# Kernel tuning notes

Measured on AMD Instinct MI355X. Metric: run time of the kernel, lower is better.

## Reference

```python
import jax, jax.numpy as jnp
import numpy as np

FEATURE_DIM = 128

def setup_inputs() -> dict:
    key0 = jax.random.key(0)
    k1, k2, k3 = jax.random.split(key0, 3)
    B, NQ, NK, D = 4, 4096, 4096, FEATURE_DIM
    return {
        "target": jax.random.normal(k1, (B, NQ, D), dtype=jnp.float32),
        "key": jax.random.normal(k2, (B, NK, D), dtype=jnp.float32),
        "value": jax.random.normal(k3, (B, NK, D), dtype=jnp.float32),
    }

def reference(target, key, value):
    # Lan_K F: scores = target @ key^T / sqrt(d); weights = softmax(scores); out = weights @ value
    scale = 1.0 / np.sqrt(FEATURE_DIM).astype(np.float32)
    scores = jnp.einsum('bqd,bkd->bqk', target, key) * scale  # [B, NQ, NK]
    weights = jax.nn.softmax(scores, axis=-1)
    return jnp.einsum('bqk,bkd->bqd', weights, value)  # [B, NQ, D]
```

## Files before the change

### kernel.cpp

```cpp
#include <hip/hip_runtime.h>
#include <stdint.h>

#define B_ 4
#define NQ_ 4096
#define NK_ 4096
#define D_ 128
#define BM_ 64
#define BN_ 128
#define NITER_ (NK_/BN_)
#define KVBUF_ 33792
#define PS_ 136
#define OS_ 66

typedef __attribute__((ext_vector_type(8))) short short8;
typedef __attribute__((ext_vector_type(4))) float floatx4;
typedef unsigned int u32;

union frag_u { u32 u[4]; short8 s; };
union pair_u { u32 u[2]; uint2 v; };

__device__ __forceinline__ unsigned short f2bf_rne(float x){
  union { float f; u32 u; } c; c.f = x;
  u32 u = c.u;
  return (unsigned short)((u + 0x7fffu + ((u >> 16) & 1u)) >> 16);
}
__device__ __forceinline__ u32 pk2bf(float a, float b){
  union { float f; u32 u; } x, y; x.f = a; y.f = b;
  return ((x.u + 0x8000u) >> 16) | ((y.u + 0x8000u) & 0xffff0000u);
}

#define GLD16(gp, lp) __builtin_amdgcn_global_load_lds( \
    (const __attribute__((address_space(1))) u32*)(gp),  \
    (__attribute__((address_space(3))) u32*)(lp), 16, 0, 0)

#define TS_ 136
__global__ void prep_kernel(const float* __restrict__ k, const float* __restrict__ v,
                            unsigned short* __restrict__ kb, unsigned short* __restrict__ vt){
  if (blockIdx.x >= 256){
    int base = (blockIdx.x - 256) * 2048 + threadIdx.x;
    #pragma unroll
    for (int i = 0; i < 8; i++){
      int j = base + i*256;
      float4 val = ((const float4*)k)[j];
      ushort4 s;
      s.x = f2bf_rne(val.x); s.y = f2bf_rne(val.y);
      s.z = f2bf_rne(val.z); s.w = f2bf_rne(val.w);
      ((ushort4*)kb)[j] = s;
    }
    return;
  }
  __shared__ __align__(16) float tile[64*TS_];
  int blk = blockIdx.x; int b = blk >> 6; int kt = blk & 63; int k0 = kt*64;
  int t = threadIdx.x;
  const float* vb = v + ((size_t)b*NK_ + k0)*D_;
  #pragma unroll
  for (int i=0;i<8;i++){
    int f = t + i*256;
    int row = f >> 5, c4 = f & 31;
    *(float4*)(tile + row*TS_ + c4*4) = *(const float4*)(vb + row*D_ + c4*4);
  }
  __syncthreads();
  unsigned short* vtb = vt + (size_t)b*D_*NK_ + k0;
  #pragma unroll
  for (int i=0;i<16;i++){
    int u2 = t + i*256;
    int d = u2 >> 5, kp = u2 & 31;
    ushort2 s2;
    s2.x = f2bf_rne(tile[(2*kp)*TS_ + d]);
    s2.y = f2bf_rne(tile[(2*kp+1)*TS_ + d]);
    *(ushort2*)(vtb + (size_t)d*NK_ + 2*kp) = s2;
  }
}

__global__ __launch_bounds__(512, 2) void attn_kernel(
    const float* __restrict__ Qf, const unsigned short* __restrict__ Kb,
    const unsigned short* __restrict__ Vt, float* __restrict__ Out){
  __shared__ __align__(16) char sm[154624];
  char* smKb = sm;
  char* smVb = sm + 2*KVBUF_;
  unsigned short* smP = (unsigned short*)(sm + 4*KVBUF_);
  float* smL = (float*)(sm + 4*KVBUF_ + 64*PS_*2);
  float* smO = (float*)sm;

  const int bi = blockIdx.x;
  const int b  = (bi >> 1) & 3;
  const int qt = ((bi >> 3) << 1) | (bi & 1);
  const int q0 = qt * BM_;
  const int tid = threadIdx.x;
  const int w = tid >> 6, lane = tid & 63;
  const int kg = w >> 1, dh = w & 1;
  const int l15 = lane & 15, l4 = lane >> 4;

  const unsigned short* kgb = Kb + (size_t)b * NK_ * D_;
  const unsigned short* vgb = Vt + (size_t)b * D_ * NK_;

  #pragma unroll
  for (int i = 0; i < 4; i++){
    int c = w*4 + i;
    { int kgc = c>>3, cp = c&7;
      int dchunk = kgc*8 + (cp&1)*4 + (cp>>1);
      const unsigned short* g = kgb + (size_t)(kgc*32 + cp*4 + (lane>>4))*D_ + (lane&15)*8;
      GLD16(g, smKb + dchunk*1056); }
    { const unsigned short* g = vgb + (size_t)(c*4 + (lane>>4))*NK_ + (lane&15)*8;
      GLD16(g, smVb + c*1056); }
  }

  short8 qf[4][4];
  {
    const float* qp = Qf + ((size_t)b*NQ_ + q0)*D_;
    #pragma unroll
    for (int nb = 0; nb < 4; nb++)
      #pragma unroll
      for (int kb = 0; kb < 4; kb++){
        const float* p = qp + (size_t)(nb*16 + l15)*D_ + kb*32 + l4*8;
        float4 a = *(const float4*)p;
        float4 c4 = *(const float4*)(p + 4);
        frag_u f;
        f.u[0] = pk2bf(a.x, a.y);  f.u[1] = pk2bf(a.z, a.w);
        f.u[2] = pk2bf(c4.x, c4.y); f.u[3] = pk2bf(c4.z, c4.w);
        qf[nb][kb] = f.s;
      }
  }

  floatx4 o[4][4];
  #pragma unroll
  for (int nb = 0; nb < 4; nb++)
    #pragma unroll
    for (int dt = 0; dt < 4; dt++) o[nb][dt] = (floatx4)0.0f;
  float lsum[4] = {0.f, 0.f, 0.f, 0.f};

  const float SL = 0.08838834764831845f * 1.4426950408889634f;

  __syncthreads();

  for (int it = 0; it < NITER_; ++it){
    const int buf = it & 1;
    char* kcur = smKb + buf * KVBUF_;
    char* vcur = smVb + buf * KVBUF_;

    if (it + 1 < NITER_){
      char* knxt = smKb + (buf ^ 1) * KVBUF_;
      #pragma unroll
      for (int i = 0; i < 4; i++){
        int c = w*4 + i;
        int kgc = c>>3, cp = c&7;
        int dchunk = kgc*8 + (cp&1)*4 + (cp>>1);
        const unsigned short* g = kgb + (size_t)((it+1)*BN_ + kgc*32 + cp*4 + (lane>>4))*D_ + (lane&15)*8;
        GLD16(g, knxt + dchunk*1056);
      }
    }

    short8 kf[4];
    {
      int row = kg*32 + dh*16 + l15;
      char* base = kcur + (row>>2)*1056 + (row&3)*256 + l4*16;
      kf[0] = *(const short8*)(base);
      kf[1] = *(const short8*)(base + 64);
      kf[2] = *(const short8*)(base + 128);
      kf[3] = *(const short8*)(base + 192);
    }
    floatx4 s[4];
    #pragma unroll
    for (int nb = 0; nb < 4; nb++){
      s[nb] = (floatx4)0.0f;
      s[nb] = __builtin_amdgcn_mfma_f32_16x16x32_bf16(kf[0], qf[nb][0], s[nb], 0,0,0);
      s[nb] = __builtin_amdgcn_mfma_f32_16x16x32_bf16(kf[1], qf[nb][1], s[nb], 0,0,0);
      s[nb] = __builtin_amdgcn_mfma_f32_16x16x32_bf16(kf[2], qf[nb][2], s[nb], 0,0,0);
      s[nb] = __builtin_amdgcn_mfma_f32_16x16x32_bf16(kf[3], qf[nb][3], s[nb], 0,0,0);
    }

    #pragma unroll
    for (int nb = 0; nb < 4; nb++){
      float p0 = __builtin_amdgcn_exp2f(s[nb][0] * SL);
      float p1 = __builtin_amdgcn_exp2f(s[nb][1] * SL);
      float p2 = __builtin_amdgcn_exp2f(s[nb][2] * SL);
      float p3 = __builtin_amdgcn_exp2f(s[nb][3] * SL);
      lsum[nb] += (p0 + p1) + (p2 + p3);
      pair_u pp; pp.u[0] = pk2bf(p0, p1); pp.u[1] = pk2bf(p2, p3);
      *(uint2*)(smP + (size_t)(nb*16 + l15)*PS_ + kg*32 + l4*8 + dh*4) = pp.v;
    }

    __syncthreads();

    if (it + 1 < NITER_){
      char* vnxt = smVb + (buf ^ 1) * KVBUF_;
      #pragma unroll
      for (int i = 0; i < 4; i++){
        int c = w*4 + i;
        const unsigned short* g = vgb + (size_t)(c*4 + (lane>>4))*NK_ + (it+1)*BN_ + (lane&15)*8;
        GLD16(g, vnxt + c*1056);
      }
    }

    short8 pf[4];
    #pragma unroll
    for (int nb = 0; nb < 4; nb++)
      pf[nb] = *(const short8*)(smP + (size_t)(nb*16 + l15)*PS_ + kg*32 + l4*8);
    short8 vf[4];
    #pragma unroll
    for (int dt = 0; dt < 4; dt++){
      int d = dh*64 + dt*16 + l15;
      vf[dt] = *(const short8*)(vcur + (d>>2)*1056 + (d&3)*256 + (kg*32 + l4*8)*2);
    }
    #pragma unroll
    for (int nb = 0; nb < 4; nb++)
      #pragma unroll
      for (int dt = 0; dt < 4; dt++)
        o[nb][dt] = __builtin_amdgcn_mfma_f32_16x16x32_bf16(pf[nb], vf[dt], o[nb][dt], 0,0,0);

    __syncthreads();
  }

  #pragma unroll
  for (int nb = 0; nb < 4; nb++){
    float v = lsum[nb];
    v += __shfl_xor(v, 16);
    v += __shfl_xor(v, 32);
    lsum[nb] = v;
  }
  if (l4 == 0)
    #pragma unroll
    for (int nb = 0; nb < 4; nb++)
      smL[w*64 + nb*16 + l15] = lsum[nb];

  if (w >= 4){
    float* r = smO + (size_t)(w - 4) * 4224;
    #pragma unroll
    for (int nb = 0; nb < 4; nb++)
      #pragma unroll
      for (int dt = 0; dt < 4; dt++)
        #pragma unroll
        for (int q = 0; q < 4; q++)
          r[(size_t)(nb*16 + l4*4 + q)*OS_ + dt*16 + l15] = o[nb][dt][q];
  }
  __syncthreads();
  if (w < 4){
    float* r = smO + (size_t)w * 4224;
    #pragma unroll
    for (int nb = 0; nb < 4; nb++)
      #pragma unroll
      for (int dt = 0; dt < 4; dt++)
        #pragma unroll
        for (int q = 0; q < 4; q++)
          o[nb][dt][q] += r[(size_t)(nb*16 + l4*4 + q)*OS_ + dt*16 + l15];
  }
  __syncthreads();
  if (w == 2 || w == 3){
    float* r = smO + (size_t)(w - 2) * 4224;
    #pragma unroll
    for (int nb = 0; nb < 4; nb++)
      #pragma unroll
      for (int dt = 0; dt < 4; dt++)
        #pragma unroll
        for (int q = 0; q < 4; q++)
          r[(size_t)(nb*16 + l4*4 + q)*OS_ + dt*16 + l15] = o[nb][dt][q];
  }
  __syncthreads();
  if (w < 2){
    float* r = smO + (size_t)w * 4224;
    float* og = Out + ((size_t)b*NQ_ + q0)*D_ + dh*64;
    #pragma unroll
    for (int nb = 0; nb < 4; nb++)
      #pragma unroll
      for (int q = 0; q < 4; q++){
        int row = nb*16 + l4*4 + q;
        float lt = 0.f;
        #pragma unroll
        for (int w2 = 0; w2 < 8; w2++) lt += smL[w2*64 + row];
        float inv = 1.0f / lt;
        #pragma unroll
        for (int dt = 0; dt < 4; dt++){
          float val = o[nb][dt][q] + r[(size_t)row*OS_ + dt*16 + l15];
          og[(size_t)row*D_ + dt*16 + l15] = val * inv;
        }
      }
  }
}

extern "C" void kernel_launch(void* const* d_in, const int* in_sizes, int n_in,
                              void* d_out, int out_size, void* d_ws, size_t ws_size,
                              hipStream_t stream){
  const float* q = (const float*)d_in[0];
  const float* k = (const float*)d_in[1];
  const float* v = (const float*)d_in[2];
  float* out = (float*)d_out;
  unsigned short* kb = (unsigned short*)d_ws;
  unsigned short* vt = kb + (size_t)B_*NK_*D_;
  prep_kernel<<<512, 256, 0, stream>>>(k, v, kb, vt);
  attn_kernel<<<256, 512, 0, stream>>>(q, kb, vt, out);
}
```

Before: 133.1 us.

## Replace padded LDS layouts with XOR-swizzled tiles and precomputed fragment offsets

Drops the padded row strides for the K/V and P shared-memory buffers and uses XOR swizzles instead, with per-thread LDS offsets precomputed outside the loop. This saves LDS space and aims to avoid bank conflicts and repeated address arithmetic in the inner loop. The prep kernel now transposes V in 128-row tiles with a swizzled staging buffer and 4-wide stores, using fewer blocks. Q conversion switches to round-to-nearest-even and P packing switches to truncation, which slightly changes numerics.

```diff
diff --git a/kernel.cpp b/kernel.cpp
--- a/kernel.cpp
+++ b/kernel.cpp
@@ -8,8 +8,7 @@
 #define BM_ 64
 #define BN_ 128
 #define NITER_ (NK_/BN_)
-#define KVBUF_ 33792
-#define PS_ 136
+#define KVBUF_ 32768
 #define OS_ 66
 
 typedef __attribute__((ext_vector_type(8))) short short8;
@@ -17,7 +16,6 @@
 typedef unsigned int u32;
 
 union frag_u { u32 u[4]; short8 s; };
-union pair_u { u32 u[2]; uint2 v; };
 
 __device__ __forceinline__ unsigned short f2bf_rne(float x){
   union { float f; u32 u; } c; c.f = x;
@@ -26,18 +24,24 @@
 }
 __device__ __forceinline__ u32 pk2bf(float a, float b){
   union { float f; u32 u; } x, y; x.f = a; y.f = b;
-  return ((x.u + 0x8000u) >> 16) | ((y.u + 0x8000u) & 0xffff0000u);
+  u32 lo = (x.u + 0x7fffu + ((x.u >> 16) & 1u)) >> 16;
+  u32 hi = (y.u + 0x7fffu + ((y.u >> 16) & 1u)) >> 16;
+  return lo | (hi << 16);
+}
+__device__ __forceinline__ u32 pk2bf_t(float a, float b){
+  union { float f; u32 u; } x, y; x.f = a; y.f = b;
+  return (x.u >> 16) | (y.u & 0xffff0000u);
 }
 
 #define GLD16(gp, lp) __builtin_amdgcn_global_load_lds( \
     (const __attribute__((address_space(1))) u32*)(gp),  \
     (__attribute__((address_space(3))) u32*)(lp), 16, 0, 0)
 
-#define TS_ 136
 __global__ void prep_kernel(const float* __restrict__ k, const float* __restrict__ v,
                             unsigned short* __restrict__ kb, unsigned short* __restrict__ vt){
-  if (blockIdx.x >= 256){
-    int base = (blockIdx.x - 256) * 2048 + threadIdx.x;
+  const int t = threadIdx.x;
+  if (blockIdx.x >= 128){
+    int base = (blockIdx.x - 128) * 2048 + t;
     #pragma unroll
     for (int i = 0; i < 8; i++){
       int j = base + i*256;
@@ -49,37 +53,39 @@
     }
     return;
   }
-  __shared__ __align__(16) float tile[64*TS_];
-  int blk = blockIdx.x; int b = blk >> 6; int kt = blk & 63; int k0 = kt*64;
-  int t = threadIdx.x;
+  __shared__ __align__(16) float tile[128*128];
+  const int b = blockIdx.x >> 5, kt = blockIdx.x & 31, k0 = kt*128;
   const float* vb = v + ((size_t)b*NK_ + k0)*D_;
   #pragma unroll
-  for (int i=0;i<8;i++){
-    int f = t + i*256;
-    int row = f >> 5, c4 = f & 31;
-    *(float4*)(tile + row*TS_ + c4*4) = *(const float4*)(vb + row*D_ + c4*4);
+  for (int i = 0; i < 16; i++){
+    int f = i*256 + t;
+    int row = f >> 5, s4 = f & 31;
+    *(float4*)(tile + row*128 + ((s4 ^ (row>>2)) << 2)) = *(const float4*)(vb + row*D_ + (s4<<2));
   }
   __syncthreads();
   unsigned short* vtb = vt + (size_t)b*D_*NK_ + k0;
   #pragma unroll
-  for (int i=0;i<16;i++){
-    int u2 = t + i*256;
-    int d = u2 >> 5, kp = u2 & 31;
-    ushort2 s2;
-    s2.x = f2bf_rne(tile[(2*kp)*TS_ + d]);
-    s2.y = f2bf_rne(tile[(2*kp+1)*TS_ + d]);
-    *(ushort2*)(vtb + (size_t)d*NK_ + 2*kp) = s2;
+  for (int i = 0; i < 16; i++){
+    int d = (t>>5) + 8*i, kq = t & 31;
+    int s4 = d >> 2, e = d & 3;
+    float v0 = tile[(4*kq+0)*128 + ((s4 ^ kq) << 2) + e];
+    float v1 = tile[(4*kq+1)*128 + ((s4 ^ kq) << 2) + e];
+    float v2 = tile[(4*kq+2)*128 + ((s4 ^ kq) << 2) + e];
+    float v3 = tile[(4*kq+3)*128 + ((s4 ^ kq) << 2) + e];
+    ushort4 o;
+    o.x = f2bf_rne(v0); o.y = f2bf_rne(v1); o.z = f2bf_rne(v2); o.w = f2bf_rne(v3);
+    *(ushort4*)(vtb + (size_t)d*NK_ + 4*kq) = o;
   }
 }
 
 __global__ __launch_bounds__(512, 2) void attn_kernel(
     const float* __restrict__ Qf, const unsigned short* __restrict__ Kb,
     const unsigned short* __restrict__ Vt, float* __restrict__ Out){
-  __shared__ __align__(16) char sm[154624];
+  __shared__ __align__(16) char sm[149504];
   char* smKb = sm;
   char* smVb = sm + 2*KVBUF_;
-  unsigned short* smP = (unsigned short*)(sm + 4*KVBUF_);
-  float* smL = (float*)(sm + 4*KVBUF_ + 64*PS_*2);
+  char* smP  = sm + 4*KVBUF_;
+  float* smL = (float*)(sm + 4*KVBUF_ + 16384);
   float* smO = (float*)sm;
 
   const int bi = blockIdx.x;
@@ -94,15 +100,15 @@
   const unsigned short* kgb = Kb + (size_t)b * NK_ * D_;
   const unsigned short* vgb = Vt + (size_t)b * D_ * NK_;
 
+  const int sr = lane >> 4;
+  const int ssl = lane & 15;
+
   #pragma unroll
   for (int i = 0; i < 4; i++){
     int c = w*4 + i;
-    { int kgc = c>>3, cp = c&7;
-      int dchunk = kgc*8 + (cp&1)*4 + (cp>>1);
-      const unsigned short* g = kgb + (size_t)(kgc*32 + cp*4 + (lane>>4))*D_ + (lane&15)*8;
-      GLD16(g, smKb + dchunk*1056); }
-    { const unsigned short* g = vgb + (size_t)(c*4 + (lane>>4))*NK_ + (lane&15)*8;
-      GLD16(g, smVb + c*1056); }
+    int sg = ssl ^ (sr + 4*(c & 1));
+    GLD16(kgb + (size_t)(c*4 + sr)*D_ + sg*8, smKb + c*1024);
+    GLD16(vgb + (size_t)(c*4 + sr)*NK_ + sg*8, smVb + c*1024);
   }
 
   short8 qf[4][4];
@@ -122,6 +128,23 @@
       }
   }
 
+  int koffs[4], voffs[4];
+  {
+    int row = kg*32 + dh*16 + l15;
+    int c = row >> 2, r = row & 3, X = r + 4*(c & 1);
+    #pragma unroll
+    for (int k = 0; k < 4; k++)
+      koffs[k] = c*1024 + r*256 + ((4*k + l4) ^ X)*16;
+  }
+  #pragma unroll
+  for (int dt = 0; dt < 4; dt++){
+    int d = dh*64 + dt*16 + l15;
+    int c = d >> 2, r = d & 3, X = r + 4*(c & 1);
+    voffs[dt] = c*1024 + r*256 + ((kg*4 + l4) ^ X)*16;
+  }
+  const int pwoff = l15*256 + (((kg*8 + dh*4 + l4) ^ (2*(l15 & 7))) * 8);
+  const int proff = l15*256 + (((kg*4 + l4) ^ (l15 & 7)) * 16);
+
   floatx4 o[4][4];
   #pragma unroll
   for (int nb = 0; nb < 4; nb++)
@@ -143,22 +166,16 @@
       #pragma unroll
       for (int i = 0; i < 4; i++){
         int c = w*4 + i;
-        int kgc = c>>3, cp = c&7;
-        int dchunk = kgc*8 + (cp&1)*4 + (cp>>1);
-        const unsigned short* g = kgb + (size_t)((it+1)*BN_ + kgc*32 + cp*4 + (lane>>4))*D_ + (lane&15)*8;
-        GLD16(g, knxt + dchunk*1056);
+        int sg = ssl ^ (sr + 4*(c & 1));
+        GLD16(kgb + (size_t)((it+1)*BN_ + c*4 + sr)*D_ + sg*8, knxt + c*1024);
       }
     }
 
     short8 kf[4];
-    {
-      int row = kg*32 + dh*16 + l15;
-      char* base = kcur + (row>>2)*1056 + (row&3)*256 + l4*16;
-      kf[0] = *(const short8*)(base);
-      kf[1] = *(const short8*)(base + 64);
-      kf[2] = *(const short8*)(base + 128);
-      kf[3] = *(const short8*)(base + 192);
-    }
+    kf[0] = *(const short8*)(kcur + koffs[0]);
+    kf[1] = *(const short8*)(kcur + koffs[1]);
+    kf[2] = *(const short8*)(kcur + koffs[2]);
+    kf[3] = *(const short8*)(kcur + koffs[3]);
     floatx4 s[4];
     #pragma unroll
     for (int nb = 0; nb < 4; nb++){
@@ -176,8 +193,8 @@
       float p2 = __builtin_amdgcn_exp2f(s[nb][2] * SL);
       float p3 = __builtin_amdgcn_exp2f(s[nb][3] * SL);
       lsum[nb] += (p0 + p1) + (p2 + p3);
-      pair_u pp; pp.u[0] = pk2bf(p0, p1); pp.u[1] = pk2bf(p2, p3);
-      *(uint2*)(smP + (size_t)(nb*16 + l15)*PS_ + kg*32 + l4*8 + dh*4) = pp.v;
+      uint2 pp; pp.x = pk2bf_t(p0, p1); pp.y = pk2bf_t(p2, p3);
+      *(uint2*)(smP + nb*4096 + pwoff) = pp;
     }
 
     __syncthreads();
@@ -187,21 +204,18 @@
       #pragma unroll
       for (int i = 0; i < 4; i++){
         int c = w*4 + i;
-        const unsigned short* g = vgb + (size_t)(c*4 + (lane>>4))*NK_ + (it+1)*BN_ + (lane&15)*8;
-        GLD16(g, vnxt + c*1056);
+        int sg = ssl ^ (sr + 4*(c & 1));
+        GLD16(vgb + (size_t)(c*4 + sr)*NK_ + (it+1)*BN_ + sg*8, vnxt + c*1024);
       }
     }
 
-    short8 pf[4];
-    #pragma unroll
-    for (int nb = 0; nb < 4; nb++)
-      pf[nb] = *(const short8*)(smP + (size_t)(nb*16 + l15)*PS_ + kg*32 + l4*8);
-    short8 vf[4];
-    #pragma unroll
-    for (int dt = 0; dt < 4; dt++){
-      int d = dh*64 + dt*16 + l15;
-      vf[dt] = *(const short8*)(vcur + (d>>2)*1056 + (d&3)*256 + (kg*32 + l4*8)*2);
-    }
+    short8 pf[4], vf[4];
+    #pragma unroll
+    for (int nb = 0; nb < 4; nb++)
+      pf[nb] = *(const short8*)(smP + nb*4096 + proff);
+    #pragma unroll
+    for (int dt = 0; dt < 4; dt++)
+      vf[dt] = *(const short8*)(vcur + voffs[dt]);
     #pragma unroll
     for (int nb = 0; nb < 4; nb++)
       #pragma unroll
@@ -286,6 +300,6 @@
   float* out = (float*)d_out;
   unsigned short* kb = (unsigned short*)d_ws;
   unsigned short* vt = kb + (size_t)B_*NK_*D_;
-  prep_kernel<<<512, 256, 0, stream>>>(k, v, kb, vt);
+  prep_kernel<<<384, 256, 0, stream>>>(k, v, kb, vt);
   attn_kernel<<<256, 512, 0, stream>>>(q, kb, vt, out);
 }
```

Measured after the change: 133.6 us. No clear change (+0.4%).
